# Kernel optimization log

Measured on AMD Instinct MI355X. Metric: run time of the kernel, lower is better.

The kernel has to match this reference:

```python
import jax, jax.numpy as jnp
import numpy as np

B, P, K = 32, 1024, 16  # clouds, points per cloud, neighbors


def setup_inputs() -> dict:
    key = jax.random.key(0)
    ks = jax.random.split(key, 5)
    N, C, H, D = B * P, 64, 128, 3
    x = jax.random.normal(ks[0], (N, C), dtype=jnp.float32)
    pos = jax.random.normal(ks[1], (N, D), dtype=jnp.float32)
    batch = jnp.arange(N, dtype=jnp.int64) // P  # cloud id per node
    W_e = jax.random.normal(ks[2], (2 * C, H), dtype=jnp.float32) * 0.05
    b_e = jnp.zeros((H,), dtype=jnp.float32)
    W_sc = jax.random.normal(ks[3], (C, H), dtype=jnp.float32) * 0.05
    b_sc = jnp.zeros((H,), dtype=jnp.float32)
    return {"x": x, "pos": pos, "batch": batch,
            "W_e": W_e, "b_e": b_e, "W_sc": W_sc, "b_sc": b_sc}


def _knn_idx(posb):
    # posb: [B, P, D] -> idx [B, P, K]: K nearest neighbors (sources) per target node,
    # within each cloud, excluding self (loop=False in torch_geometric.knn_graph).
    sq = jnp.sum(posb * posb, axis=-1)                       # [B, P]
    d2 = sq[:, :, None] + sq[:, None, :] - 2.0 * jnp.einsum('bid,bjd->bij', posb, posb)
    d2 = d2 + jnp.eye(P, dtype=posb.dtype)[None] * jnp.finfo(posb.dtype).max / 2
    _, idx = jax.lax.top_k(-d2, K)                           # [B, P, K]
    return idx


def reference(x, pos, batch, W_e, b_e, W_sc, b_sc):
    C = x.shape[-1]
    xb = x.reshape(B, P, C)
    posb = pos.reshape(B, P, -1)
    idx = _knn_idx(posb)                                     # [B, P, K]
    # gather neighbor (source) features per target node
    x_j = jax.vmap(lambda xc, ic: xc[ic])(xb, idx)           # [B, P, K, C]
    x_i = xb[:, :, None, :]                                  # [B, P, 1, C]
    # EdgeConv message: nn([x_i, x_j - x_i]), here Linear + ReLU
    e = jnp.concatenate([jnp.broadcast_to(x_i, x_j.shape), x_j - x_i], axis=-1)  # [B,P,K,2C]
    msg = jax.nn.relu(jnp.einsum('bpke,eh->bpkh', e, W_e) + b_e)
    agg = jnp.max(msg, axis=2)                               # max aggregation -> [B, P, H]
    shortcut = x @ W_sc + b_sc                               # [N, H]
    out = agg.reshape(-1, agg.shape[-1]) + shortcut
    return out
```

## Files before the change

### kernel.cpp

```cpp
#include <hip/hip_runtime.h>
#include <float.h>
#include <stdint.h>

#define BATCHES 32
#define P 1024
#define KNN 16
#define C 64
#define H 128
#define N (BATCHES * P)
#define NCOLS 384
#define SPLITS 8
#define CPS 128
#define QB 32
#define PADH 132

typedef short short8 __attribute__((ext_vector_type(8)));
typedef float floatx4 __attribute__((ext_vector_type(4)));

__device__ __forceinline__ unsigned short f2bf(float f) {
    unsigned u = __float_as_uint(f);
    unsigned r = (u + 0x7FFF + ((u >> 16) & 1)) >> 16;
    return (unsigned short)r;
}

__global__ __launch_bounds__(256) void prep_w(
    const float* __restrict__ W_e, const float* __restrict__ b_e,
    const float* __restrict__ W_sc, const float* __restrict__ b_sc,
    unsigned short* __restrict__ WT, float* __restrict__ bias)
{
    int i = blockIdx.x * 256 + threadIdx.x;
    int col = i >> 6, c = i & 63;
    float w;
    if (col < 128)      w = W_e[c * 128 + col] - W_e[(64 + c) * 128 + col];
    else if (col < 256) w = W_e[(64 + c) * 128 + (col - 128)];
    else                w = W_sc[c * 128 + (col - 256)];
    WT[col * 64 + c] = f2bf(w);
    if (c == 0) {
        bias[col] = (col < 128) ? b_e[col] : (col < 256 ? 0.0f : b_sc[col - 256]);
    }
}

struct alignas(16) F4 { float x, y, z, w; };

struct PA {
    F4    spos[P + 8];
    float lists[SPLITS][16][QB];
    unsigned short offs[SPLITS][QB];
    unsigned short cnts[SPLITS][QB];
    float Tq[QB];
};
struct PB {
    unsigned short Ubuf[QB][PADH];
    unsigned short Vbuf[QB][PADH];
    unsigned short Sbuf[QB][PADH];
};

__global__ __launch_bounds__(256, 4) void knn_gemm_kernel(
    const float* __restrict__ pos, const float* __restrict__ X,
    const unsigned short* __restrict__ WT, const float* __restrict__ bias,
    int* __restrict__ idx_out,
    unsigned short* __restrict__ U, unsigned short* __restrict__ V,
    unsigned short* __restrict__ S)
{
    __shared__ __align__(16) char smraw[sizeof(PA)];
    PA* A  = (PA*)smraw;
    PB* Bm = (PB*)smraw;

    int t = threadIdx.x;
    int q = t & 31, s = t >> 5;
    int blk = blockIdx.x;
    int batch = blk >> 5;
    int qblk  = blk & 31;
    int iloc  = qblk * QB + q;

    const float* pb = pos + (size_t)batch * P * 3;
    for (int j = t; j < P; j += 256) {
        float x = pb[j * 3 + 0], y = pb[j * 3 + 1], z = pb[j * 3 + 2];
        float sq = __fadd_rn(__fadd_rn(__fmul_rn(x, x), __fmul_rn(y, y)),
                             __fmul_rn(z, z));
        A->spos[j] = F4{x, y, z, sq};
    }
    __syncthreads();

    F4 me = A->spos[iloc];
    const int j0 = s * CPS;

    float d[16];
#pragma unroll
    for (int k = 0; k < 16; ++k) d[k] = FLT_MAX;

    auto dist = [&](const F4& c, int j) -> float {
        float dot = __fadd_rn(__fadd_rn(__fmul_rn(me.x, c.x), __fmul_rn(me.y, c.y)),
                              __fmul_rn(me.z, c.z));
        float d2 = __fadd_rn(__fadd_rn(me.w, c.w), __fmul_rn(-2.0f, dot));
        return (j == iloc) ? FLT_MAX : d2;
    };
    auto insert = [&](float d2) {
#pragma unroll
        for (int k = 15; k >= 1; --k)
            d[k] = __builtin_amdgcn_fmed3f(d[k - 1], d2, d[k]);
        d[0] = fminf(d[0], d2);
    };

#pragma unroll 8
    for (int jj = 0; jj < CPS; ++jj) {
        int j = j0 + jj;
        F4 c = A->spos[j];
        insert(dist(c, j));
    }

#pragma unroll
    for (int k = 0; k < 16; ++k) A->lists[s][k][q] = d[k];
    __syncthreads();

    if ((t >> 6) == (blk & 3) && (t & 63) < 32) {
        float v[8], wv[8];
        int   n[8];
#pragma unroll
        for (int l = 0; l < 8; ++l) {
            v[l]  = A->lists[l][0][q];
            wv[l] = A->lists[l][1][q];
            n[l]  = 0;
        }
        float T = 0.0f;
#pragma unroll 1
        for (int k = 0; k < 16; ++k) {
            float mn = fminf(fminf(fminf(v[0], v[1]), fminf(v[2], v[3])),
                             fminf(fminf(v[4], v[5]), fminf(v[6], v[7])));
            bool taken = false;
#pragma unroll
            for (int l = 0; l < 8; ++l) {
                bool tk = (!taken) && (v[l] == mn);
                taken = taken || tk;
                int ni = n[l] + (tk ? 1 : 0);
                int ri = ni + 1;
                float rv = A->lists[l][(ri < 16) ? ri : 15][q];
                float wnew = (ri < 16) ? rv : FLT_MAX;
                v[l]  = tk ? wv[l] : v[l];
                wv[l] = tk ? wnew  : wv[l];
                n[l]  = ni;
            }
            T = mn;
        }
        A->Tq[q] = T;
        int off = 0;
#pragma unroll
        for (int l = 0; l < 8; ++l) {
            A->offs[l][q] = (unsigned short)off;
            A->cnts[l][q] = (unsigned short)n[l];
            off += n[l];
        }
    }
    __syncthreads();

    {
        float T  = A->Tq[q];
        int   cap = A->cnts[s][q];
        int   gb  = (blk * QB + q) * KNN + A->offs[s][q];
        int   base = batch * P;
        int   cnt = 0;

#pragma unroll 4
        for (int jj = 0; jj < CPS; ++jj) {
            int j = j0 + jj;
            F4 c = A->spos[j];
            float d2 = dist(c, j);
            if (d2 <= T && cnt < cap) {
                idx_out[gb + cnt] = base + j;
                cnt++;
            }
        }
    }
    __syncthreads();

    {
        int w  = t >> 6;
        int ln = t & 63;
        int mt = w & 1, nh = w >> 1;
        int m0 = blk * QB + mt * 16;
        int lm = ln & 15, kg = ln >> 4;

        const float4* arow = (const float4*)(X + (size_t)(m0 + lm) * 64 + kg * 8);
        float4 f0 = arow[0], f1 = arow[1];
        float4 f2 = arow[8], f3 = arow[9];
        short8 a0, a1;
        a0[0] = (short)f2bf(f0.x); a0[1] = (short)f2bf(f0.y);
        a0[2] = (short)f2bf(f0.z); a0[3] = (short)f2bf(f0.w);
        a0[4] = (short)f2bf(f1.x); a0[5] = (short)f2bf(f1.y);
        a0[6] = (short)f2bf(f1.z); a0[7] = (short)f2bf(f1.w);
        a1[0] = (short)f2bf(f2.x); a1[1] = (short)f2bf(f2.y);
        a1[2] = (short)f2bf(f2.z); a1[3] = (short)f2bf(f2.w);
        a1[4] = (short)f2bf(f3.x); a1[5] = (short)f2bf(f3.y);
        a1[6] = (short)f2bf(f3.z); a1[7] = (short)f2bf(f3.w);

#pragma unroll 4
        for (int nt = nh * 12; nt < nh * 12 + 12; ++nt) {
            const short8* brow = (const short8*)(WT + (size_t)(nt * 16 + lm) * 64 + kg * 8);
            short8 b0 = brow[0];
            short8 b1 = brow[4];
            floatx4 acc = {0.0f, 0.0f, 0.0f, 0.0f};
            acc = __builtin_amdgcn_mfma_f32_16x16x32_bf16(a0, b0, acc, 0, 0, 0);
            acc = __builtin_amdgcn_mfma_f32_16x16x32_bf16(a1, b1, acc, 0, 0, 0);

            int col = nt * 16 + lm;
            float bv = bias[col];
#pragma unroll
            for (int r = 0; r < 4; ++r) {
                int row = mt * 16 + kg * 4 + r;
                unsigned short val = f2bf(acc[r] + bv);
                if (col < 128)      Bm->Ubuf[row][col] = val;
                else if (col < 256) Bm->Vbuf[row][col - 128] = val;
                else                Bm->Sbuf[row][col - 256] = val;
            }
        }
    }
    __syncthreads();

    {
        uint2* Ug = (uint2*)U + (size_t)blk * 1024;
        uint2* Vg = (uint2*)V + (size_t)blk * 1024;
        uint2* Sg = (uint2*)S + (size_t)blk * 1024;
#pragma unroll
        for (int i = t; i < 1024; i += 256) {
            int row = i >> 5, off = (i & 31) * 4;
            Ug[i] = *(const uint2*)&Bm->Ubuf[row][off];
            Vg[i] = *(const uint2*)&Bm->Vbuf[row][off];
            Sg[i] = *(const uint2*)&Bm->Sbuf[row][off];
        }
    }
}

__global__ __launch_bounds__(256) void final_kernel(
    const int* __restrict__ idx, const unsigned short* __restrict__ U,
    const unsigned short* __restrict__ V, const unsigned short* __restrict__ S,
    float* __restrict__ out)
{
    int t = threadIdx.x;
    __shared__ int nbr[16][KNN];
    ((int*)nbr)[t] = idx[(size_t)blockIdx.x * 256 + t];
    __syncthreads();

    int pl = t >> 4;
    int c8 = t & 15;
    size_t p = (size_t)blockIdx.x * 16 + pl;

    uint4 uu = ((const uint4*)(U + p * H))[c8];
    uint4 ss = ((const uint4*)(S + p * H))[c8];

    float m0 = -FLT_MAX, m1 = -FLT_MAX, m2 = -FLT_MAX, m3 = -FLT_MAX;
    float m4 = -FLT_MAX, m5 = -FLT_MAX, m6 = -FLT_MAX, m7 = -FLT_MAX;
#pragma unroll
    for (int k = 0; k < KNN; ++k) {
        int row = nbr[pl][k];
        uint4 vv = *(const uint4*)(V + (size_t)row * H + c8 * 8);
        m0 = fmaxf(m0, __uint_as_float(vv.x << 16));
        m1 = fmaxf(m1, __uint_as_float(vv.x & 0xFFFF0000u));
        m2 = fmaxf(m2, __uint_as_float(vv.y << 16));
        m3 = fmaxf(m3, __uint_as_float(vv.y & 0xFFFF0000u));
        m4 = fmaxf(m4, __uint_as_float(vv.z << 16));
        m5 = fmaxf(m5, __uint_as_float(vv.z & 0xFFFF0000u));
        m6 = fmaxf(m6, __uint_as_float(vv.w << 16));
        m7 = fmaxf(m7, __uint_as_float(vv.w & 0xFFFF0000u));
    }

    float4 oa, ob;
    oa.x = fmaxf(__uint_as_float(uu.x << 16)         + m0, 0.0f) + __uint_as_float(ss.x << 16);
    oa.y = fmaxf(__uint_as_float(uu.x & 0xFFFF0000u) + m1, 0.0f) + __uint_as_float(ss.x & 0xFFFF0000u);
    oa.z = fmaxf(__uint_as_float(uu.y << 16)         + m2, 0.0f) + __uint_as_float(ss.y << 16);
    oa.w = fmaxf(__uint_as_float(uu.y & 0xFFFF0000u) + m3, 0.0f) + __uint_as_float(ss.y & 0xFFFF0000u);
    ob.x = fmaxf(__uint_as_float(uu.z << 16)         + m4, 0.0f) + __uint_as_float(ss.z << 16);
    ob.y = fmaxf(__uint_as_float(uu.z & 0xFFFF0000u) + m5, 0.0f) + __uint_as_float(ss.z & 0xFFFF0000u);
    ob.z = fmaxf(__uint_as_float(uu.w << 16)         + m6, 0.0f) + __uint_as_float(ss.w << 16);
    ob.w = fmaxf(__uint_as_float(uu.w & 0xFFFF0000u) + m7, 0.0f) + __uint_as_float(ss.w & 0xFFFF0000u);
    ((float4*)(out + p * H))[c8 * 2]     = oa;
    ((float4*)(out + p * H))[c8 * 2 + 1] = ob;
}

extern "C" void kernel_launch(void* const* d_in, const int* in_sizes, int n_in,
                              void* d_out, int out_size, void* d_ws, size_t ws_size,
                              hipStream_t stream)
{
    const float* x    = (const float*)d_in[0];
    const float* pos  = (const float*)d_in[1];
    const float* W_e  = (const float*)d_in[3];
    const float* b_e  = (const float*)d_in[4];
    const float* W_sc = (const float*)d_in[5];
    const float* b_sc = (const float*)d_in[6];
    float* out = (float*)d_out;

    char* ws = (char*)d_ws;
    const size_t OFF_IDX  = 0;
    const size_t OFF_U    = 2ull << 20;
    const size_t OFF_V    = OFF_U + (8ull << 20);
    const size_t OFF_S    = OFF_V + (8ull << 20);
    const size_t OFF_WT   = OFF_S + (8ull << 20);
    const size_t OFF_BIAS = OFF_WT + 49152;

    int*            idx  = (int*)(ws + OFF_IDX);
    unsigned short* U    = (unsigned short*)(ws + OFF_U);
    unsigned short* V    = (unsigned short*)(ws + OFF_V);
    unsigned short* S    = (unsigned short*)(ws + OFF_S);
    unsigned short* WT   = (unsigned short*)(ws + OFF_WT);
    float*          bias = (float*)(ws + OFF_BIAS);

    prep_w<<<(NCOLS * C) / 256, 256, 0, stream>>>(W_e, b_e, W_sc, b_sc, WT, bias);
    knn_gemm_kernel<<<N / QB, 256, 0, stream>>>(pos, x, WT, bias, idx, U, V, S);
    final_kernel<<<N / 16, 256, 0, stream>>>(idx, U, V, S, out);
}
```

Measured before the change: 142.6 us.

## Precompute packed positions globally, drop LDS staging to raise occupancy

Result: slower. 159.2 us (+11.6%).

```diff
diff --git a/kernel.cpp b/kernel.cpp
--- a/kernel.cpp
+++ b/kernel.cpp
@@ -12,10 +12,11 @@
 #define SPLITS 8
 #define CPS 128
 #define QB 32
-#define PADH 132
 
 typedef short short8 __attribute__((ext_vector_type(8)));
 typedef float floatx4 __attribute__((ext_vector_type(4)));
+
+struct alignas(16) F4 { float x, y, z, w; };
 
 __device__ __forceinline__ unsigned short f2bf(float f) {
     unsigned u = __float_as_uint(f);
@@ -23,48 +24,50 @@
     return (unsigned short)r;
 }
 
-__global__ __launch_bounds__(256) void prep_w(
+__global__ __launch_bounds__(256) void prep_kernel(
     const float* __restrict__ W_e, const float* __restrict__ b_e,
     const float* __restrict__ W_sc, const float* __restrict__ b_sc,
-    unsigned short* __restrict__ WT, float* __restrict__ bias)
-{
-    int i = blockIdx.x * 256 + threadIdx.x;
-    int col = i >> 6, c = i & 63;
-    float w;
-    if (col < 128)      w = W_e[c * 128 + col] - W_e[(64 + c) * 128 + col];
-    else if (col < 256) w = W_e[(64 + c) * 128 + (col - 128)];
-    else                w = W_sc[c * 128 + (col - 256)];
-    WT[col * 64 + c] = f2bf(w);
-    if (c == 0) {
-        bias[col] = (col < 128) ? b_e[col] : (col < 256 ? 0.0f : b_sc[col - 256]);
-    }
-}
-
-struct alignas(16) F4 { float x, y, z, w; };
+    const float* __restrict__ pos,
+    unsigned short* __restrict__ WT, float* __restrict__ bias,
+    F4* __restrict__ posq)
+{
+    int b = blockIdx.x;
+    if (b < 96) {
+        int i = b * 256 + threadIdx.x;
+        int col = i >> 6, c = i & 63;
+        float w;
+        if (col < 128)      w = W_e[c * 128 + col] - W_e[(64 + c) * 128 + col];
+        else if (col < 256) w = W_e[(64 + c) * 128 + (col - 128)];
+        else                w = W_sc[c * 128 + (col - 256)];
+        WT[col * 64 + c] = f2bf(w);
+        if (c == 0) {
+            bias[col] = (col < 128) ? b_e[col] : (col < 256 ? 0.0f : b_sc[col - 256]);
+        }
+    } else {
+        int j = (b - 96) * 256 + threadIdx.x;
+        float x = pos[j * 3 + 0], y = pos[j * 3 + 1], z = pos[j * 3 + 2];
+        float sq = __fadd_rn(__fadd_rn(__fmul_rn(x, x), __fmul_rn(y, y)),
+                             __fmul_rn(z, z));
+        posq[j] = F4{x, y, z, sq};
+    }
+}
 
 struct PA {
-    F4    spos[P + 8];
     float lists[SPLITS][16][QB];
     unsigned short offs[SPLITS][QB];
     unsigned short cnts[SPLITS][QB];
     float Tq[QB];
 };
-struct PB {
-    unsigned short Ubuf[QB][PADH];
-    unsigned short Vbuf[QB][PADH];
-    unsigned short Sbuf[QB][PADH];
-};
-
-__global__ __launch_bounds__(256, 4) void knn_gemm_kernel(
-    const float* __restrict__ pos, const float* __restrict__ X,
+
+__global__ __launch_bounds__(256, 8) void knn_gemm_kernel(
+    const F4* __restrict__ posq, const float* __restrict__ X,
     const unsigned short* __restrict__ WT, const float* __restrict__ bias,
     int* __restrict__ idx_out,
     unsigned short* __restrict__ U, unsigned short* __restrict__ V,
     unsigned short* __restrict__ S)
 {
-    __shared__ __align__(16) char smraw[sizeof(PA)];
-    PA* A  = (PA*)smraw;
-    PB* Bm = (PB*)smraw;
+    __shared__ __align__(16) PA Ash;
+    PA* A = &Ash;
 
     int t = threadIdx.x;
     int q = t & 31, s = t >> 5;
@@ -73,16 +76,8 @@
     int qblk  = blk & 31;
     int iloc  = qblk * QB + q;
 
-    const float* pb = pos + (size_t)batch * P * 3;
-    for (int j = t; j < P; j += 256) {
-        float x = pb[j * 3 + 0], y = pb[j * 3 + 1], z = pb[j * 3 + 2];
-        float sq = __fadd_rn(__fadd_rn(__fmul_rn(x, x), __fmul_rn(y, y)),
-                             __fmul_rn(z, z));
-        A->spos[j] = F4{x, y, z, sq};
-    }
-    __syncthreads();
-
-    F4 me = A->spos[iloc];
+    const F4* pq = posq + (size_t)batch * P;
+    F4 me = pq[iloc];
     const int j0 = s * CPS;
 
     float d[16];
@@ -102,10 +97,10 @@
         d[0] = fminf(d[0], d2);
     };
 
-#pragma unroll 8
+#pragma unroll 4
     for (int jj = 0; jj < CPS; ++jj) {
         int j = j0 + jj;
-        F4 c = A->spos[j];
+        F4 c = pq[j];
         insert(dist(c, j));
     }
 
@@ -163,7 +158,7 @@
 #pragma unroll 4
         for (int jj = 0; jj < CPS; ++jj) {
             int j = j0 + jj;
-            F4 c = A->spos[j];
+            F4 c = pq[j];
             float d2 = dist(c, j);
             if (d2 <= T && cnt < cap) {
                 idx_out[gb + cnt] = base + j;
@@ -171,7 +166,6 @@
             }
         }
     }
-    __syncthreads();
 
     {
         int w  = t >> 6;
@@ -193,6 +187,8 @@
         a1[4] = (short)f2bf(f3.x); a1[5] = (short)f2bf(f3.y);
         a1[6] = (short)f2bf(f3.z); a1[7] = (short)f2bf(f3.w);
 
+        size_t rowbase = (size_t)(blk * QB + mt * 16 + kg * 4) * H;
+
 #pragma unroll 4
         for (int nt = nh * 12; nt < nh * 12 + 12; ++nt) {
             const short8* brow = (const short8*)(WT + (size_t)(nt * 16 + lm) * 64 + kg * 8);
@@ -204,28 +200,12 @@
 
             int col = nt * 16 + lm;
             float bv = bias[col];
-#pragma unroll
-            for (int r = 0; r < 4; ++r) {
-                int row = mt * 16 + kg * 4 + r;
-                unsigned short val = f2bf(acc[r] + bv);
-                if (col < 128)      Bm->Ubuf[row][col] = val;
-                else if (col < 256) Bm->Vbuf[row][col - 128] = val;
-                else                Bm->Sbuf[row][col - 256] = val;
-            }
-        }
-    }
-    __syncthreads();
-
-    {
-        uint2* Ug = (uint2*)U + (size_t)blk * 1024;
-        uint2* Vg = (uint2*)V + (size_t)blk * 1024;
-        uint2* Sg = (uint2*)S + (size_t)blk * 1024;
-#pragma unroll
-        for (int i = t; i < 1024; i += 256) {
-            int row = i >> 5, off = (i & 31) * 4;
-            Ug[i] = *(const uint2*)&Bm->Ubuf[row][off];
-            Vg[i] = *(const uint2*)&Bm->Vbuf[row][off];
-            Sg[i] = *(const uint2*)&Bm->Sbuf[row][off];
+            unsigned short* dst = (col < 128) ? (U + col)
+                                : (col < 256) ? (V + (col - 128))
+                                              : (S + (col - 256));
+#pragma unroll
+            for (int r = 0; r < 4; ++r)
+                dst[rowbase + (size_t)r * H] = f2bf(acc[r] + bv);
         }
     }
 }
@@ -295,6 +275,7 @@
     const size_t OFF_S    = OFF_V + (8ull << 20);
     const size_t OFF_WT   = OFF_S + (8ull << 20);
     const size_t OFF_BIAS = OFF_WT + 49152;
+    const size_t OFF_POSQ = OFF_BIAS + 2048;
 
     int*            idx  = (int*)(ws + OFF_IDX);
     unsigned short* U    = (unsigned short*)(ws + OFF_U);
@@ -302,8 +283,10 @@
     unsigned short* S    = (unsigned short*)(ws + OFF_S);
     unsigned short* WT   = (unsigned short*)(ws + OFF_WT);
     float*          bias = (float*)(ws + OFF_BIAS);
-
-    prep_w<<<(NCOLS * C) / 256, 256, 0, stream>>>(W_e, b_e, W_sc, b_sc, WT, bias);
-    knn_gemm_kernel<<<N / QB, 256, 0, stream>>>(pos, x, WT, bias, idx, U, V, S);
+    F4*             posq = (F4*)(ws + OFF_POSQ);
+
+    prep_kernel<<<96 + N / 256, 256, 0, stream>>>(W_e, b_e, W_sc, b_sc, pos,
+                                                  WT, bias, posq);
+    knn_gemm_kernel<<<N / QB, 256, 0, stream>>>(posq, x, WT, bias, idx, U, V, S);
     final_kernel<<<N / 16, 256, 0, stream>>>(idx, U, V, S, out);
 }
```

## Move V GEMM into prep kernel and fuse gather-max into kNN kernel

Applied to the files above, without the earlier changes.

New measurement: 132.5 us. 7.1% less time.

```diff
diff --git a/kernel.cpp b/kernel.cpp
--- a/kernel.cpp
+++ b/kernel.cpp
@@ -8,14 +8,15 @@
 #define C 64
 #define H 128
 #define N (BATCHES * P)
-#define NCOLS 384
 #define SPLITS 8
 #define CPS 128
 #define QB 32
-#define PADH 132
+#define PADH 136
 
 typedef short short8 __attribute__((ext_vector_type(8)));
 typedef float floatx4 __attribute__((ext_vector_type(4)));
+
+struct alignas(16) F4 { float x, y, z, w; };
 
 __device__ __forceinline__ unsigned short f2bf(float f) {
     unsigned u = __float_as_uint(f);
@@ -23,48 +24,104 @@
     return (unsigned short)r;
 }
 
-__global__ __launch_bounds__(256) void prep_w(
+__global__ __launch_bounds__(256) void prep_kernel(
     const float* __restrict__ W_e, const float* __restrict__ b_e,
     const float* __restrict__ W_sc, const float* __restrict__ b_sc,
-    unsigned short* __restrict__ WT, float* __restrict__ bias)
+    const float* __restrict__ X,
+    unsigned short* __restrict__ WT, float* __restrict__ bias,
+    unsigned short* __restrict__ V)
 {
-    int i = blockIdx.x * 256 + threadIdx.x;
-    int col = i >> 6, c = i & 63;
-    float w;
-    if (col < 128)      w = W_e[c * 128 + col] - W_e[(64 + c) * 128 + col];
-    else if (col < 256) w = W_e[(64 + c) * 128 + (col - 128)];
-    else                w = W_sc[c * 128 + (col - 256)];
-    WT[col * 64 + c] = f2bf(w);
-    if (c == 0) {
-        bias[col] = (col < 128) ? b_e[col] : (col < 256 ? 0.0f : b_sc[col - 256]);
+    __shared__ unsigned short Vs[128][PADH];
+    int b = blockIdx.x;
+    int t = threadIdx.x;
+    if (b < 96) {
+        int i = b * 256 + t;
+        int col = i >> 6, c = i & 63;
+        float w;
+        if (col < 128)      w = W_e[c * 128 + col] - W_e[(64 + c) * 128 + col];
+        else if (col < 256) w = W_e[(64 + c) * 128 + (col - 128)];
+        else                w = W_sc[c * 128 + (col - 256)];
+        WT[col * 64 + c] = f2bf(w);
+        if (c == 0) {
+            bias[col] = (col < 128) ? b_e[col] : (col < 256 ? 0.0f : b_sc[col - 256]);
+        }
+        return;
+    }
+
+    int vb = b - 96;
+    int m0 = vb * 128;
+    int w  = t >> 6, ln = t & 63;
+    int lm = ln & 15, kg = ln >> 4;
+
+    short8 a0[2], a1[2];
+#pragma unroll
+    for (int i = 0; i < 2; ++i) {
+        int row = m0 + (2 * w + i) * 16 + lm;
+        const float4* ar = (const float4*)(X + (size_t)row * 64 + kg * 8);
+        float4 f0 = ar[0], f1 = ar[1], f2 = ar[8], f3 = ar[9];
+        a0[i][0] = (short)f2bf(f0.x); a0[i][1] = (short)f2bf(f0.y);
+        a0[i][2] = (short)f2bf(f0.z); a0[i][3] = (short)f2bf(f0.w);
+        a0[i][4] = (short)f2bf(f1.x); a0[i][5] = (short)f2bf(f1.y);
+        a0[i][6] = (short)f2bf(f1.z); a0[i][7] = (short)f2bf(f1.w);
+        a1[i][0] = (short)f2bf(f2.x); a1[i][1] = (short)f2bf(f2.y);
+        a1[i][2] = (short)f2bf(f2.z); a1[i][3] = (short)f2bf(f2.w);
+        a1[i][4] = (short)f2bf(f3.x); a1[i][5] = (short)f2bf(f3.y);
+        a1[i][6] = (short)f2bf(f3.z); a1[i][7] = (short)f2bf(f3.w);
+    }
+
+#pragma unroll 2
+    for (int ct = 0; ct < 8; ++ct) {
+        int col = ct * 16 + lm;
+        short8 b0, b1;
+#pragma unroll
+        for (int i = 0; i < 8; ++i) {
+            b0[i] = (short)f2bf(W_e[(size_t)(64 + kg * 8 + i) * 128 + col]);
+            b1[i] = (short)f2bf(W_e[(size_t)(96 + kg * 8 + i) * 128 + col]);
+        }
+#pragma unroll
+        for (int i = 0; i < 2; ++i) {
+            floatx4 acc = {0.0f, 0.0f, 0.0f, 0.0f};
+            acc = __builtin_amdgcn_mfma_f32_16x16x32_bf16(a0[i], b0, acc, 0, 0, 0);
+            acc = __builtin_amdgcn_mfma_f32_16x16x32_bf16(a1[i], b1, acc, 0, 0, 0);
+#pragma unroll
+            for (int r = 0; r < 4; ++r)
+                Vs[(2 * w + i) * 16 + kg * 4 + r][col] = f2bf(acc[r]);
+        }
+    }
+    __syncthreads();
+
+    uint2* Vg = (uint2*)V + (size_t)vb * 4096;
+#pragma unroll
+    for (int i = t; i < 4096; i += 256) {
+        int row = i >> 5, off = (i & 31) * 4;
+        Vg[i] = *(const uint2*)&Vs[row][off];
     }
 }
 
-struct alignas(16) F4 { float x, y, z, w; };
-
-struct PA {
-    F4    spos[P + 8];
-    float lists[SPLITS][16][QB];
-    unsigned short offs[SPLITS][QB];
-    unsigned short cnts[SPLITS][QB];
-    float Tq[QB];
-};
-struct PB {
-    unsigned short Ubuf[QB][PADH];
-    unsigned short Vbuf[QB][PADH];
-    unsigned short Sbuf[QB][PADH];
+struct SM {
+    F4 spos[P + 8];
+    union {
+        struct {
+            float lists[SPLITS][16][QB];
+            unsigned short offs[SPLITS][QB];
+            unsigned short cnts[SPLITS][QB];
+            float Tq[QB];
+        };
+        struct {
+            unsigned short Ubuf[QB][PADH];
+            unsigned short Sbuf[QB][PADH];
+        };
+    };
+    int nbr[QB][KNN];
 };
 
 __global__ __launch_bounds__(256, 4) void knn_gemm_kernel(
     const float* __restrict__ pos, const float* __restrict__ X,
     const unsigned short* __restrict__ WT, const float* __restrict__ bias,
-    int* __restrict__ idx_out,
-    unsigned short* __restrict__ U, unsigned short* __restrict__ V,
-    unsigned short* __restrict__ S)
+    const unsigned short* __restrict__ V,
+    float* __restrict__ out)
 {
-    __shared__ __align__(16) char smraw[sizeof(PA)];
-    PA* A  = (PA*)smraw;
-    PB* Bm = (PB*)smraw;
+    __shared__ __align__(16) SM A;
 
     int t = threadIdx.x;
     int q = t & 31, s = t >> 5;
@@ -78,11 +135,11 @@
         float x = pb[j * 3 + 0], y = pb[j * 3 + 1], z = pb[j * 3 + 2];
         float sq = __fadd_rn(__fadd_rn(__fmul_rn(x, x), __fmul_rn(y, y)),
                              __fmul_rn(z, z));
-        A->spos[j] = F4{x, y, z, sq};
-    }
-    __syncthreads();
-
-    F4 me = A->spos[iloc];
+        A.spos[j] = F4{x, y, z, sq};
+    }
+    __syncthreads();
+
+    F4 me = A.spos[iloc];
     const int j0 = s * CPS;
 
     float d[16];
@@ -105,21 +162,22 @@
 #pragma unroll 8
     for (int jj = 0; jj < CPS; ++jj) {
         int j = j0 + jj;
-        F4 c = A->spos[j];
+        F4 c = A.spos[j];
         insert(dist(c, j));
     }
 
 #pragma unroll
-    for (int k = 0; k < 16; ++k) A->lists[s][k][q] = d[k];
-    __syncthreads();
-
-    if ((t >> 6) == (blk & 3) && (t & 63) < 32) {
+    for (int k = 0; k < 16; ++k) A.lists[s][k][q] = d[k];
+    __syncthreads();
+
+    if ((t >> 6) == (blk & 3) && (t & 63) < QB) {
+        int qm = t & 63;
         float v[8], wv[8];
         int   n[8];
 #pragma unroll
         for (int l = 0; l < 8; ++l) {
-            v[l]  = A->lists[l][0][q];
-            wv[l] = A->lists[l][1][q];
+            v[l]  = A.lists[l][0][qm];
+            wv[l] = A.lists[l][1][qm];
             n[l]  = 0;
         }
         float T = 0.0f;
@@ -134,7 +192,7 @@
                 taken = taken || tk;
                 int ni = n[l] + (tk ? 1 : 0);
                 int ri = ni + 1;
-                float rv = A->lists[l][(ri < 16) ? ri : 15][q];
+                float rv = A.lists[l][(ri < 16) ? ri : 15][qm];
                 float wnew = (ri < 16) ? rv : FLT_MAX;
                 v[l]  = tk ? wv[l] : v[l];
                 wv[l] = tk ? wnew  : wv[l];
@@ -142,31 +200,31 @@
             }
             T = mn;
         }
-        A->Tq[q] = T;
+        A.Tq[qm] = T;
         int off = 0;
 #pragma unroll
         for (int l = 0; l < 8; ++l) {
-            A->offs[l][q] = (unsigned short)off;
-            A->cnts[l][q] = (unsigned short)n[l];
+            A.offs[l][qm] = (unsigned short)off;
+            A.cnts[l][qm] = (unsigned short)n[l];
             off += n[l];
         }
     }
     __syncthreads();
 
     {
-        float T  = A->Tq[q];
-        int   cap = A->cnts[s][q];
-        int   gb  = (blk * QB + q) * KNN + A->offs[s][q];
+        float T  = A.Tq[q];
+        int   cap = A.cnts[s][q];
+        int   ob  = A.offs[s][q];
         int   base = batch * P;
         int   cnt = 0;
 
 #pragma unroll 4
         for (int jj = 0; jj < CPS; ++jj) {
             int j = j0 + jj;
-            F4 c = A->spos[j];
+            F4 c = A.spos[j];
             float d2 = dist(c, j);
             if (d2 <= T && cnt < cap) {
-                idx_out[gb + cnt] = base + j;
+                A.nbr[q][ob + cnt] = base + j;
                 cnt++;
             }
         }
@@ -193,8 +251,9 @@
         a1[4] = (short)f2bf(f3.x); a1[5] = (short)f2bf(f3.y);
         a1[6] = (short)f2bf(f3.z); a1[7] = (short)f2bf(f3.w);
 
+        int tbase = (nh == 0) ? 0 : 16;
 #pragma unroll 4
-        for (int nt = nh * 12; nt < nh * 12 + 12; ++nt) {
+        for (int nt = tbase; nt < tbase + 8; ++nt) {
             const short8* brow = (const short8*)(WT + (size_t)(nt * 16 + lm) * 64 + kg * 8);
             short8 b0 = brow[0];
             short8 b1 = brow[4];
@@ -208,72 +267,53 @@
             for (int r = 0; r < 4; ++r) {
                 int row = mt * 16 + kg * 4 + r;
                 unsigned short val = f2bf(acc[r] + bv);
-                if (col < 128)      Bm->Ubuf[row][col] = val;
-                else if (col < 256) Bm->Vbuf[row][col - 128] = val;
-                else                Bm->Sbuf[row][col - 256] = val;
+                if (col < 128) A.Ubuf[row][col] = val;
+                else           A.Sbuf[row][col - 256] = val;
             }
         }
     }
     __syncthreads();
 
     {
-        uint2* Ug = (uint2*)U + (size_t)blk * 1024;
-        uint2* Vg = (uint2*)V + (size_t)blk * 1024;
-        uint2* Sg = (uint2*)S + (size_t)blk * 1024;
-#pragma unroll
-        for (int i = t; i < 1024; i += 256) {
-            int row = i >> 5, off = (i & 31) * 4;
-            Ug[i] = *(const uint2*)&Bm->Ubuf[row][off];
-            Vg[i] = *(const uint2*)&Bm->Vbuf[row][off];
-            Sg[i] = *(const uint2*)&Bm->Sbuf[row][off];
-        }
-    }
-}
-
-__global__ __launch_bounds__(256) void final_kernel(
-    const int* __restrict__ idx, const unsigned short* __restrict__ U,
-    const unsigned short* __restrict__ V, const unsigned short* __restrict__ S,
-    float* __restrict__ out)
-{
-    int t = threadIdx.x;
-    __shared__ int nbr[16][KNN];
-    ((int*)nbr)[t] = idx[(size_t)blockIdx.x * 256 + t];
-    __syncthreads();
-
-    int pl = t >> 4;
-    int c8 = t & 15;
-    size_t p = (size_t)blockIdx.x * 16 + pl;
-
-    uint4 uu = ((const uint4*)(U + p * H))[c8];
-    uint4 ss = ((const uint4*)(S + p * H))[c8];
-
-    float m0 = -FLT_MAX, m1 = -FLT_MAX, m2 = -FLT_MAX, m3 = -FLT_MAX;
-    float m4 = -FLT_MAX, m5 = -FLT_MAX, m6 = -FLT_MAX, m7 = -FLT_MAX;
-#pragma unroll
-    for (int k = 0; k < KNN; ++k) {
-        int row = nbr[pl][k];
-        uint4 vv = *(const uint4*)(V + (size_t)row * H + c8 * 8);
-        m0 = fmaxf(m0, __uint_as_float(vv.x << 16));
-        m1 = fmaxf(m1, __uint_as_float(vv.x & 0xFFFF0000u));
-        m2 = fmaxf(m2, __uint_as_float(vv.y << 16));
-        m3 = fmaxf(m3, __uint_as_float(vv.y & 0xFFFF0000u));
-        m4 = fmaxf(m4, __uint_as_float(vv.z << 16));
-        m5 = fmaxf(m5, __uint_as_float(vv.z & 0xFFFF0000u));
-        m6 = fmaxf(m6, __uint_as_float(vv.w << 16));
-        m7 = fmaxf(m7, __uint_as_float(vv.w & 0xFFFF0000u));
-    }
-
-    float4 oa, ob;
-    oa.x = fmaxf(__uint_as_float(uu.x << 16)         + m0, 0.0f) + __uint_as_float(ss.x << 16);
-    oa.y = fmaxf(__uint_as_float(uu.x & 0xFFFF0000u) + m1, 0.0f) + __uint_as_float(ss.x & 0xFFFF0000u);
-    oa.z = fmaxf(__uint_as_float(uu.y << 16)         + m2, 0.0f) + __uint_as_float(ss.y << 16);
-    oa.w = fmaxf(__uint_as_float(uu.y & 0xFFFF0000u) + m3, 0.0f) + __uint_as_float(ss.y & 0xFFFF0000u);
-    ob.x = fmaxf(__uint_as_float(uu.z << 16)         + m4, 0.0f) + __uint_as_float(ss.z << 16);
-    ob.y = fmaxf(__uint_as_float(uu.z & 0xFFFF0000u) + m5, 0.0f) + __uint_as_float(ss.z & 0xFFFF0000u);
-    ob.z = fmaxf(__uint_as_float(uu.w << 16)         + m6, 0.0f) + __uint_as_float(ss.w << 16);
-    ob.w = fmaxf(__uint_as_float(uu.w & 0xFFFF0000u) + m7, 0.0f) + __uint_as_float(ss.w & 0xFFFF0000u);
-    ((float4*)(out + p * H))[c8 * 2]     = oa;
-    ((float4*)(out + p * H))[c8 * 2 + 1] = ob;
+        int pl = t >> 4;
+        int c8 = t & 15;
+#pragma unroll
+        for (int half = 0; half < 2; ++half) {
+            int q2 = half * 16 + pl;
+            size_t p = (size_t)blk * QB + q2;
+
+            uint4 uu = *(const uint4*)&A.Ubuf[q2][c8 * 8];
+            uint4 ss = *(const uint4*)&A.Sbuf[q2][c8 * 8];
+
+            float m0 = -FLT_MAX, m1 = -FLT_MAX, m2 = -FLT_MAX, m3 = -FLT_MAX;
+            float m4 = -FLT_MAX, m5 = -FLT_MAX, m6 = -FLT_MAX, m7 = -FLT_MAX;
+#pragma unroll
+            for (int k = 0; k < KNN; ++k) {
+                int row = A.nbr[q2][k];
+                uint4 vv = *(const uint4*)(V + (size_t)row * H + c8 * 8);
+                m0 = fmaxf(m0, __uint_as_float(vv.x << 16));
+                m1 = fmaxf(m1, __uint_as_float(vv.x & 0xFFFF0000u));
+                m2 = fmaxf(m2, __uint_as_float(vv.y << 16));
+                m3 = fmaxf(m3, __uint_as_float(vv.y & 0xFFFF0000u));
+                m4 = fmaxf(m4, __uint_as_float(vv.z << 16));
+                m5 = fmaxf(m5, __uint_as_float(vv.z & 0xFFFF0000u));
+                m6 = fmaxf(m6, __uint_as_float(vv.w << 16));
+                m7 = fmaxf(m7, __uint_as_float(vv.w & 0xFFFF0000u));
+            }
+
+            float4 oa, ob;
+            oa.x = fmaxf(__uint_as_float(uu.x << 16)         + m0, 0.0f) + __uint_as_float(ss.x << 16);
+            oa.y = fmaxf(__uint_as_float(uu.x & 0xFFFF0000u) + m1, 0.0f) + __uint_as_float(ss.x & 0xFFFF0000u);
+            oa.z = fmaxf(__uint_as_float(uu.y << 16)         + m2, 0.0f) + __uint_as_float(ss.y << 16);
+            oa.w = fmaxf(__uint_as_float(uu.y & 0xFFFF0000u) + m3, 0.0f) + __uint_as_float(ss.y & 0xFFFF0000u);
+            ob.x = fmaxf(__uint_as_float(uu.z << 16)         + m4, 0.0f) + __uint_as_float(ss.z << 16);
+            ob.y = fmaxf(__uint_as_float(uu.z & 0xFFFF0000u) + m5, 0.0f) + __uint_as_float(ss.z & 0xFFFF0000u);
+            ob.z = fmaxf(__uint_as_float(uu.w << 16)         + m6, 0.0f) + __uint_as_float(ss.w << 16);
+            ob.w = fmaxf(__uint_as_float(uu.w & 0xFFFF0000u) + m7, 0.0f) + __uint_as_float(ss.w & 0xFFFF0000u);
+            ((float4*)(out + p * H))[c8 * 2]     = oa;
+            ((float4*)(out + p * H))[c8 * 2 + 1] = ob;
+        }
+    }
 }
 
 extern "C" void kernel_launch(void* const* d_in, const int* in_sizes, int n_in,
@@ -289,21 +329,15 @@
     float* out = (float*)d_out;
 
     char* ws = (char*)d_ws;
-    const size_t OFF_IDX  = 0;
-    const size_t OFF_U    = 2ull << 20;
-    const size_t OFF_V    = OFF_U + (8ull << 20);
-    const size_t OFF_S    = OFF_V + (8ull << 20);
-    const size_t OFF_WT   = OFF_S + (8ull << 20);
+    const size_t OFF_V    = 0;
+    const size_t OFF_WT   = 8ull << 20;
     const size_t OFF_BIAS = OFF_WT + 49152;
 
-    int*            idx  = (int*)(ws + OFF_IDX);
-    unsigned short* U    = (unsigned short*)(ws + OFF_U);
     unsigned short* V    = (unsigned short*)(ws + OFF_V);
-    unsigned short* S    = (unsigned short*)(ws + OFF_S);
     unsigned short* WT   = (unsigned short*)(ws + OFF_WT);
     float*          bias = (float*)(ws + OFF_BIAS);
 
-    prep_w<<<(NCOLS * C) / 256, 256, 0, stream>>>(W_e, b_e, W_sc, b_sc, WT, bias);
-    knn_gemm_kernel<<<N / QB, 256, 0, stream>>>(pos, x, WT, bias, idx, U, V, S);
-    final_kernel<<<N / 16, 256, 0, stream>>>(idx, U, V, S, out);
+    prep_kernel<<<96 + N / 128, 256, 0, stream>>>(W_e, b_e, W_sc, b_sc, x,
+                                                  WT, bias, V);
+    knn_gemm_kernel<<<N / QB, 256, 0, stream>>>(pos, x, WT, bias, V, out);
 }
```
